# Optimization experiments

Measured on AMD Instinct MI355X. Metric: run time of the kernel, lower is better.

## Reference

```python
import jax, jax.numpy as jnp
import numpy as np


def setup_inputs() -> dict:
    key = jax.random.key(0)
    # Head output: [batch, grid_h, grid_w, anchors, 5] = (x, y, w, h, score)
    # scores ~ U[0,1] so ~half the boxes pass the 0.5 threshold.
    X = jax.random.uniform(key, (128, 64, 64, 9, 5), dtype=jnp.float32)
    score_threshold = jnp.ones((1,), dtype=jnp.float32) * 0.5
    return {"X": X, "score_threshold": score_threshold}


def reference(X, score_threshold):
    # Faithful jax version of: reshape(-1,5); keep boxes with score>thr;
    # convert xywh -> xyxy. The torch code does a Python loop + stack
    # (variable-length compaction); in jax we compute the keep-mask and
    # the converted coords for all boxes, zeroing dropped ones, and
    # return the mask so downstream compaction is a prefix-sum away.
    boxes = X.reshape(-1, 5)                       # [N, 5]
    keep = boxes[:, 4] > score_threshold[0]        # [N] bool
    xy = boxes[:, 0:2]                             # centers
    half_wh = boxes[:, 2:4] * 0.5
    xyxy = jnp.concatenate([xy - half_wh, xy + half_wh], axis=-1)  # [N, 4]
    out = jnp.where(keep[:, None], xyxy, jnp.zeros((), dtype=xyxy.dtype))
    return out, keep
```

## Files before the change

kernel.cpp:

```cpp
#include <hip/hip_runtime.h>


__global__ __launch_bounds__(256) void plate_kernel(
    const float* __restrict__ X,
    const float* __restrict__ thr_p,
    float* __restrict__ out_xyxy,
    float* __restrict__ out_keep,
    int nquads)
{
    int t = blockIdx.x * blockDim.x + threadIdx.x;
    if (t >= nquads) return;

    const float thr = thr_p[0];

    const float4* __restrict__ src = reinterpret_cast<const float4*>(X) + (size_t)t * 5;
    float f[20];
    #pragma unroll
    for (int i = 0; i < 5; ++i) {
        float4 v = src[i];
        f[i * 4 + 0] = v.x;
        f[i * 4 + 1] = v.y;
        f[i * 4 + 2] = v.z;
        f[i * 4 + 3] = v.w;
    }

    float4 res[4];
    float  kf[4];
    #pragma unroll
    for (int b = 0; b < 4; ++b) {
        float x = f[b * 5 + 0];
        float y = f[b * 5 + 1];
        float w = f[b * 5 + 2];
        float h = f[b * 5 + 3];
        float s = f[b * 5 + 4];
        bool keep = s > thr;
        float hw = w * 0.5f;
        float hh = h * 0.5f;
        float4 r;
        r.x = keep ? (x - hw) : 0.0f;
        r.y = keep ? (y - hh) : 0.0f;
        r.z = keep ? (x + hw) : 0.0f;
        r.w = keep ? (y + hh) : 0.0f;
        res[b] = r;
        kf[b]  = keep ? 1.0f : 0.0f;
    }

    float4* __restrict__ dst = reinterpret_cast<float4*>(out_xyxy) + (size_t)t * 4;
    #pragma unroll
    for (int b = 0; b < 4; ++b) dst[b] = res[b];

    reinterpret_cast<float4*>(out_keep)[t] = make_float4(kf[0], kf[1], kf[2], kf[3]);
}

extern "C" void kernel_launch(void* const* d_in, const int* in_sizes, int n_in,
                              void* d_out, int out_size, void* d_ws, size_t ws_size,
                              hipStream_t stream)
{
    const float* X   = (const float*)d_in[0];
    const float* thr = (const float*)d_in[1];

    const long long n_boxes = (long long)in_sizes[0] / 5;
    const int nquads = (int)(n_boxes / 4);

    float* out_xyxy = (float*)d_out;
    float* out_keep = (float*)d_out + n_boxes * 4;

    const int block = 256;
    const int grid  = (nquads + block - 1) / block;

    plate_kernel<<<grid, block, 0, stream>>>(X, thr, out_xyxy, out_keep, nquads);
}
```

Measured before the change: 35.36 us.

## Stage box tiles through LDS for coalesced loads and stores, use nontemporal stores

Each block now loads a tile of 1024 boxes into shared memory with fully coalesced float4 reads, synchronises, then each thread processes boxes at stride 256. In the old layout each thread read 80 contiguous bytes and wrote 64, so adjacent lanes were strided apart. The new path writes xyxy as coalesced float4s and keep flags as coalesced scalars, all with nontemporal hints. It costs 20KB of LDS per block, a barrier, and stride-5 LDS reads that may hit bank conflicts. It assumes the box count is a multiple of 1024.

```diff
diff --git a/kernel.cpp b/kernel.cpp
--- a/kernel.cpp
+++ b/kernel.cpp
@@ -1,55 +1,52 @@
 #include <hip/hip_runtime.h>
 
+
+using f4 = __attribute__((ext_vector_type(4))) float;
 
 __global__ __launch_bounds__(256) void plate_kernel(
     const float* __restrict__ X,
     const float* __restrict__ thr_p,
     float* __restrict__ out_xyxy,
     float* __restrict__ out_keep,
-    int nquads)
+    int ntiles)
 {
-    int t = blockIdx.x * blockDim.x + threadIdx.x;
-    if (t >= nquads) return;
+    __shared__ float lds[5120];
 
+    const int tile = blockIdx.x;
+    if (tile >= ntiles) return;
+    const int j = threadIdx.x;
     const float thr = thr_p[0];
 
-    const float4* __restrict__ src = reinterpret_cast<const float4*>(X) + (size_t)t * 5;
-    float f[20];
+    const f4* __restrict__ src = reinterpret_cast<const f4*>(X) + (size_t)tile * 1280;
+    f4* __restrict__ ldsv = reinterpret_cast<f4*>(lds);
     #pragma unroll
-    for (int i = 0; i < 5; ++i) {
-        float4 v = src[i];
-        f[i * 4 + 0] = v.x;
-        f[i * 4 + 1] = v.y;
-        f[i * 4 + 2] = v.z;
-        f[i * 4 + 3] = v.w;
-    }
+    for (int k = 0; k < 5; ++k)
+        ldsv[k * 256 + j] = src[k * 256 + j];
 
-    float4 res[4];
-    float  kf[4];
+    __syncthreads();
+
+    f4*    __restrict__ dst = reinterpret_cast<f4*>(out_xyxy) + (size_t)tile * 1024;
+    float* __restrict__ kp  = out_keep + (size_t)tile * 1024;
+
     #pragma unroll
-    for (int b = 0; b < 4; ++b) {
-        float x = f[b * 5 + 0];
-        float y = f[b * 5 + 1];
-        float w = f[b * 5 + 2];
-        float h = f[b * 5 + 3];
-        float s = f[b * 5 + 4];
-        bool keep = s > thr;
-        float hw = w * 0.5f;
-        float hh = h * 0.5f;
-        float4 r;
+    for (int k = 0; k < 4; ++k) {
+        const int m = k * 256 + j;
+        const float x = lds[5 * m + 0];
+        const float y = lds[5 * m + 1];
+        const float w = lds[5 * m + 2];
+        const float h = lds[5 * m + 3];
+        const float s = lds[5 * m + 4];
+        const bool keep = s > thr;
+        const float hw = w * 0.5f;
+        const float hh = h * 0.5f;
+        f4 r;
         r.x = keep ? (x - hw) : 0.0f;
         r.y = keep ? (y - hh) : 0.0f;
         r.z = keep ? (x + hw) : 0.0f;
         r.w = keep ? (y + hh) : 0.0f;
-        res[b] = r;
-        kf[b]  = keep ? 1.0f : 0.0f;
+        __builtin_nontemporal_store(r, &dst[m]);
+        __builtin_nontemporal_store(keep ? 1.0f : 0.0f, &kp[m]);
     }
-
-    float4* __restrict__ dst = reinterpret_cast<float4*>(out_xyxy) + (size_t)t * 4;
-    #pragma unroll
-    for (int b = 0; b < 4; ++b) dst[b] = res[b];
-
-    reinterpret_cast<float4*>(out_keep)[t] = make_float4(kf[0], kf[1], kf[2], kf[3]);
 }
 
 extern "C" void kernel_launch(void* const* d_in, const int* in_sizes, int n_in,
@@ -60,13 +57,10 @@
     const float* thr = (const float*)d_in[1];
 
     const long long n_boxes = (long long)in_sizes[0] / 5;
-    const int nquads = (int)(n_boxes / 4);
+    const int ntiles = (int)(n_boxes / 1024);
 
     float* out_xyxy = (float*)d_out;
     float* out_keep = (float*)d_out + n_boxes * 4;
 
-    const int block = 256;
-    const int grid  = (nquads + block - 1) / block;
-
-    plate_kernel<<<grid, block, 0, stream>>>(X, thr, out_xyxy, out_keep, nquads);
+    plate_kernel<<<ntiles, 256, 0, stream>>>(X, thr, out_xyxy, out_keep, ntiles);
 }
```

Result: faster. 32.75 us (-7.4%).
